# Kernel tuning notes

Measured on AMD Instinct MI355X. Metric: run time of the kernel, lower is better.

The kernel has to match this reference:

```python
import jax, jax.numpy as jnp
import numpy as np

# 5x5 neighborhood offsets as (dx, dy), row-major as in the original delta list
DELTA = [(dx, dy) for dy in (-2, -1, 0, 1, 2) for dx in (-2, -1, 0, 1, 2)]
BN_EPS = 1e-5


def _conv(x, w, padding):
    return jax.lax.conv_general_dilated(
        x, w, window_strides=(1, 1), padding=padding,
        dimension_numbers=('NCHW', 'OIHW', 'NCHW'))


def setup_inputs() -> dict:
    key = jax.random.key(0)
    ks = jax.random.split(key, 4)
    B, C, H, W = 128, 256, 24, 24
    source_feature = jax.random.normal(ks[0], (B, C, H, W), jnp.float32)
    detection_feature = jax.random.normal(ks[1], (B, C, H, W), jnp.float32)
    w1 = jax.random.normal(ks[2], (256, 512, 3, 3), jnp.float32) * 0.02
    b1 = jnp.zeros((256,), jnp.float32)
    bn_gamma = jnp.ones((256,), jnp.float32)
    bn_beta = jnp.zeros((256,), jnp.float32)
    bn_mean = jnp.zeros((256,), jnp.float32)
    bn_var = jnp.ones((256,), jnp.float32)
    w2 = jax.random.normal(ks[3], (25, 256, 1, 1), jnp.float32) * 0.05
    b2 = jnp.zeros((25,), jnp.float32)
    return dict(source_feature=source_feature, detection_feature=detection_feature,
                w1=w1, b1=b1, bn_gamma=bn_gamma, bn_beta=bn_beta,
                bn_mean=bn_mean, bn_var=bn_var, w2=w2, b2=b2)


def reference(source_feature, detection_feature, w1, b1, bn_gamma, bn_beta,
              bn_mean, bn_var, w2, b2):
    B, C, H, W = source_feature.shape
    # kernel_pre: Conv3x3(512->256, pad 1) + BN + ReLU + Conv1x1(256->25)
    concat_f = jnp.concatenate([source_feature, detection_feature], axis=1)  # [B,512,H,W]
    x = _conv(concat_f, w1, ((1, 1), (1, 1))) + b1[None, :, None, None]
    inv = bn_gamma / jnp.sqrt(bn_var + BN_EPS)
    x = x * inv[None, :, None, None] + (bn_beta - bn_mean * inv)[None, :, None, None]
    x = jax.nn.relu(x)
    logits = _conv(x, w2, ((0, 0), (0, 0))) + b2[None, :, None, None]  # [B,25,H,W]
    # per-pixel softmax over the 25 neighborhood taps
    kmaps = jax.nn.softmax(logits, axis=1)  # [B,25,H,W]
    # propagate: softmax-weighted 5x5 neighbor gather-sum; out-of-bounds taps
    # contribute zero (matches the skipped-boundary terms in the original loop)
    padded = jnp.pad(source_feature, ((0, 0), (0, 0), (2, 2), (2, 2)))
    prop = jnp.zeros_like(source_feature)
    for order, (dx, dy) in enumerate(DELTA):
        shifted = padded[:, :, 2 + dy:2 + dy + H, 2 + dx:2 + dx + W]  # [B,C,H,W]
        prop = prop + shifted * kmaps[:, order][:, None]  # broadcast over C
    return prop
```

## Files before the change

### kernel.cpp

```cpp
#include <hip/hip_runtime.h>
#include <hip/hip_bf16.h>
#include <stdint.h>

#define BATCH 128
#define CIN   256
#define CCAT  512
#define HH    24
#define WW    24
#define HP    26
#define WP    26
#define COUT  256
#define KDIM  4608
#define NPIX  576
#define MDIM  73728
#define NORD  25

typedef __attribute__((ext_vector_type(8))) short bf16x8;
typedef __attribute__((ext_vector_type(4))) float f32x4;

__device__ __forceinline__ unsigned short f2bf(float v) {
    union { float f; unsigned u; } x; x.f = v;
    unsigned r = x.u + 0x7fffu + ((x.u >> 16) & 1u);
    return (unsigned short)(r >> 16);
}
__device__ __forceinline__ float bf_lo(unsigned w) {
    union { unsigned u; float f; } x; x.u = w << 16; return x.f;
}
__device__ __forceinline__ float bf_hi(unsigned w) {
    union { unsigned u; float f; } x; x.u = w & 0xffff0000u; return x.f;
}

__device__ __forceinline__ void async_copy16(const void* gsrc, void* ldst) {
    __builtin_amdgcn_global_load_lds(
        (const __attribute__((address_space(1))) unsigned int*)gsrc,
        (__attribute__((address_space(3))) unsigned int*)ldst, 16, 0, 0);
}

#define PTILE 192
#define LSTR  72
__global__ __launch_bounds__(256) void prep_transpose(
        const float* __restrict__ src, const float* __restrict__ det,
        unsigned short* __restrict__ apad) {
    __shared__ unsigned short lds[PTILE * LSTR];
    int pt = blockIdx.x;
    int cg = blockIdx.y;
    int b  = blockIdx.z;
    int c0 = cg * 64;
    int p0 = pt * PTILE;
    const float* inp = (c0 < CIN)
        ? (src + ((long)b * CIN + c0) * NPIX)
        : (det + ((long)b * CIN + (c0 - CIN)) * NPIX);
    int tid = threadIdx.x;

    #pragma unroll
    for (int it = 0; it < 12; it++) {
        int l  = it * 256 + tid;
        int cq = l / PTILE;
        int px = l - cq * PTILE;
        const float* pb = inp + (long)cq * 4 * NPIX + p0 + px;
        unsigned short v0 = f2bf(pb[0 * NPIX]);
        unsigned short v1 = f2bf(pb[1 * NPIX]);
        unsigned short v2 = f2bf(pb[2 * NPIX]);
        unsigned short v3 = f2bf(pb[3 * NPIX]);
        uint2 w;
        w.x = (unsigned)v0 | ((unsigned)v1 << 16);
        w.y = (unsigned)v2 | ((unsigned)v3 << 16);
        *(uint2*)&lds[px * LSTR + cq * 4] = w;
    }
    __syncthreads();

    #pragma unroll
    for (int it = 0; it < 6; it++) {
        int l   = it * 256 + tid;
        int px  = l >> 3;
        int ch8 = l & 7;
        uint4 w = *(const uint4*)&lds[px * LSTR + ch8 * 8];
        int p  = p0 + px;
        int y  = p / WW, x = p - y * WW;
        long o = (((long)b * HP + (y + 1)) * WP + (x + 1)) * CCAT + c0 + ch8 * 8;
        *(uint4*)(apad + o) = w;
    }
}

__global__ __launch_bounds__(256) void zero_halo(unsigned short* __restrict__ apad) {
    int t = blockIdx.x * 256 + threadIdx.x;
    int ch8 = t & 63;
    int r   = t >> 6;
    int hp  = r % 100;
    int b   = r / 100;
    int y, x;
    if (hp < 26)      { y = 0;       x = hp; }
    else if (hp < 52) { y = 25;      x = hp - 26; }
    else if (hp < 76) { y = hp - 51; x = 0; }
    else              { y = hp - 75; x = 25; }
    long o = (((long)b * HP + y) * WP + x) * CCAT + ch8 * 8;
    *(uint4*)(apad + o) = (uint4){0u, 0u, 0u, 0u};
}

__global__ __launch_bounds__(256) void prep_w(
        const float* __restrict__ w1, const float* __restrict__ b1,
        const float* __restrict__ gam, const float* __restrict__ bet,
        const float* __restrict__ mu, const float* __restrict__ var,
        unsigned short* __restrict__ bt,
        float* __restrict__ scale, float* __restrict__ shift) {
    int idx = blockIdx.x * 256 + threadIdx.x;
    if (idx < COUT * KDIM) {
        int n = idx / KDIM;
        int k = idx - n * KDIM;
        int s = k >> 9;
        int ci = k & 511;
        int ky = s / 3, kx = s - ky * 3;
        float v = w1[(((long)n * 512 + ci) * 3 + ky) * 3 + kx];
        bt[idx] = f2bf(v);
    }
    if (blockIdx.x == 0 && threadIdx.x < COUT) {
        int c = threadIdx.x;
        float inv = gam[c] * rsqrtf(var[c] + 1e-5f);
        scale[c] = inv;
        shift[c] = (b1[c] - mu[c]) * inv + bet[c];
    }
}

#define BUF_SH  34816
#define ABUF_SH 18432
#define STAGE_A(j, nb, soff) \
    async_copy16(apad + aSrc[j] + (soff), (void*)&lds[(nb)*BUF_SH + (j)*4096 + w*512])
#define STAGE_B(j, nb, koff) \
    async_copy16(bt + bSrc[j] + (koff), (void*)&lds[(nb)*BUF_SH + ABUF_SH + (j)*4096 + w*512])
#define BAR()  __builtin_amdgcn_s_barrier()
#define WAITV4() { asm volatile("s_waitcnt vmcnt(4)" ::: "memory"); }
#define WAITV0() { asm volatile("s_waitcnt vmcnt(0)" ::: "memory"); }
#define WAITL()  { asm volatile("s_waitcnt lgkmcnt(0)" ::: "memory"); __builtin_amdgcn_sched_barrier(0); }

#define AFRAGS(mh, csw) { \
    _Pragma("unroll") \
    for (int m = 0; m < 3; m++) \
        afr[m] = *(const bf16x8*)(L + aBase + ((mh) * 3 + m) * 2048 + (csw)); }
#define BFRAGS(csw) { \
    _Pragma("unroll") \
    for (int n = 0; n < 4; n++) \
        bfr[n] = *(const bf16x8*)(L + bBase + n * 2048 + (csw)); }
#define DOMFMA(mh) { \
    __builtin_amdgcn_s_setprio(1); \
    _Pragma("unroll") \
    for (int m = 0; m < 3; m++) \
        _Pragma("unroll") \
        for (int n = 0; n < 4; n++) \
            acc[(mh) * 3 + m][n] = __builtin_amdgcn_mfma_f32_16x16x32_bf16( \
                afr[m], bfr[n], acc[(mh) * 3 + m][n], 0, 0, 0); \
    __builtin_amdgcn_s_setprio(0); }

__global__ __launch_bounds__(512, 2) void conv1_gemm(
        const unsigned short* __restrict__ apad,
        const unsigned short* __restrict__ bt,
        const float* __restrict__ scale, const float* __restrict__ shift,
        unsigned short* __restrict__ xout) {
    __shared__ unsigned short lds[2 * BUF_SH];
    const int tid  = threadIdx.x;
    const int w    = tid >> 6;
    const int lane = tid & 63;
    const int wr = w >> 2, wc = w & 3;
    const int fr = lane & 15, ls = lane >> 4;
    const long m0 = (long)blockIdx.x * 288;

    const int rowq = tid >> 3;
    const int sl   = (tid & 7) ^ (rowq & 7);
    long aSrc[5], bSrc[4];
    #pragma unroll
    for (int j = 0; j < 5; j++) {
        int r = (j == 4) ? (256 + (rowq & 31)) : (j * 64 + rowq);
        long m = m0 + r;
        int b  = (int)(m / NPIX);
        int rr = (int)(m - (long)b * NPIX);
        int y = rr / WW, x = rr - y * WW;
        aSrc[j] = (((long)b * HP + y) * WP + x) * (long)CCAT + sl * 8;
    }
    #pragma unroll
    for (int j = 0; j < 4; j++)
        bSrc[j] = (long)(j * 64 + rowq) * KDIM + sl * 8;

    const int rb   = fr & 7;
    const int csw0 = ((ls    ) ^ rb) << 4;
    const int csw1 = ((ls + 4) ^ rb) << 4;
    const int aBase = (wr * 144 + fr) * 128;
    const int bBase = ABUF_SH * 2 + (wc * 64 + fr) * 128;

    f32x4 acc[9][4];
    #pragma unroll
    for (int i = 0; i < 9; i++)
        #pragma unroll
        for (int j = 0; j < 4; j++) acc[i][j] = (f32x4){0.f, 0.f, 0.f, 0.f};

    STAGE_B(0, 0, 0); STAGE_B(1, 0, 0); STAGE_B(2, 0, 0); STAGE_B(3, 0, 0);
    STAGE_A(0, 0, 0); STAGE_A(1, 0, 0); STAGE_A(2, 0, 0); STAGE_A(3, 0, 0);
    if (tid < 256) STAGE_A(4, 0, 0);

    bf16x8 afr[3], bfr[4];
    int nb = 0;
    for (int kt = 0; kt < 71; kt++) {
        const int ktn = kt + 1;
        const int seg = ktn >> 3;
        const int ky = seg / 3, kx = seg - ky * 3;
        const long soff = (long)(ky * WP + kx) * CCAT + (ktn & 7) * 64;
        const long koff = (long)ktn * 64;
        const int pb = nb ^ 1;
        const char* L = (const char*)lds + nb * (BUF_SH * 2);

        STAGE_B(0, pb, koff); STAGE_B(1, pb, koff);
        STAGE_B(2, pb, koff); STAGE_B(3, pb, koff);
        WAITV4();
        BAR();
        BFRAGS(csw0); AFRAGS(0, csw0);
        WAITL();
        DOMFMA(0);
        BAR();

        AFRAGS(1, csw0);
        STAGE_A(0, pb, soff); STAGE_A(1, pb, soff);
        WAITL();
        DOMFMA(1);
        BAR();

        AFRAGS(2, csw0);
        STAGE_A(2, pb, soff); STAGE_A(3, pb, soff);
        if (tid < 256) STAGE_A(4, pb, soff);
        WAITL();
        DOMFMA(2);
        BAR();

        BFRAGS(csw1); AFRAGS(0, csw1);
        WAITL();
        DOMFMA(0);
        BAR();

        AFRAGS(1, csw1);
        WAITL();
        DOMFMA(1);
        BAR();

        AFRAGS(2, csw1);
        WAITL();
        DOMFMA(2);
        BAR();

        nb ^= 1;
    }

    {
        const char* L = (const char*)lds + nb * (BUF_SH * 2);
        WAITV0();
        BAR();
        BFRAGS(csw0); AFRAGS(0, csw0); WAITL(); DOMFMA(0);
        AFRAGS(1, csw0);               WAITL(); DOMFMA(1);
        AFRAGS(2, csw0);               WAITL(); DOMFMA(2);
        BFRAGS(csw1); AFRAGS(0, csw1); WAITL(); DOMFMA(0);
        AFRAGS(1, csw1);               WAITL(); DOMFMA(1);
        AFRAGS(2, csw1);               WAITL(); DOMFMA(2);
    }

    #pragma unroll
    for (int n = 0; n < 4; n++) {
        int col = wc * 64 + n * 16 + fr;
        float sc = scale[col], sh = shift[col];
        #pragma unroll
        for (int m = 0; m < 9; m++) {
            long rbase = m0 + wr * 144 + m * 16 + ls * 4;
            #pragma unroll
            for (int j = 0; j < 4; j++) {
                float v = acc[m][n][j] * sc + sh;
                v = v > 0.f ? v : 0.f;
                xout[(rbase + j) * COUT + col] = f2bf(v);
            }
        }
    }
}

__global__ __launch_bounds__(256) void conv2_softmax(
        const unsigned short* __restrict__ x, const float* __restrict__ w2,
        const float* __restrict__ b2, float* __restrict__ kmaps) {
    __shared__ float w2s[NORD * 256];
    __shared__ float b2s[NORD];
    for (int i = threadIdx.x; i < NORD * 256; i += 256) w2s[i] = w2[i];
    if (threadIdx.x < NORD) b2s[threadIdx.x] = b2[threadIdx.x];
    __syncthreads();
    long pix = (long)blockIdx.x * 256 + threadIdx.x;
    float acc[NORD];
    #pragma unroll
    for (int o = 0; o < NORD; o++) acc[o] = b2s[o];
    const unsigned short* xr = x + pix * COUT;
    for (int kc = 0; kc < 32; kc++) {
        uint4 raw = *(const uint4*)(xr + kc * 8);
        float xf[8];
        xf[0] = bf_lo(raw.x); xf[1] = bf_hi(raw.x);
        xf[2] = bf_lo(raw.y); xf[3] = bf_hi(raw.y);
        xf[4] = bf_lo(raw.z); xf[5] = bf_hi(raw.z);
        xf[6] = bf_lo(raw.w); xf[7] = bf_hi(raw.w);
        #pragma unroll
        for (int o = 0; o < NORD; o++) {
            const float* wrow = &w2s[o * 256 + kc * 8];
            float4 wa = *(const float4*)(wrow);
            float4 wb = *(const float4*)(wrow + 4);
            acc[o] += xf[0] * wa.x + xf[1] * wa.y + xf[2] * wa.z + xf[3] * wa.w
                    + xf[4] * wb.x + xf[5] * wb.y + xf[6] * wb.z + xf[7] * wb.w;
        }
    }
    float mx = acc[0];
    #pragma unroll
    for (int o = 1; o < NORD; o++) mx = fmaxf(mx, acc[o]);
    float s = 0.f;
    #pragma unroll
    for (int o = 0; o < NORD; o++) { acc[o] = expf(acc[o] - mx); s += acc[o]; }
    float inv = 1.f / s;
    #pragma unroll
    for (int o = 0; o < NORD; o++) kmaps[(long)o * MDIM + pix] = acc[o] * inv;
}

__global__ __launch_bounds__(576) void propagate(
        const float* __restrict__ src, const float* __restrict__ kmaps,
        float* __restrict__ out) {
    __shared__ float sm[4][28 * 28];
    int b  = blockIdx.y;
    int cg = blockIdx.x;
    int tid = threadIdx.x;
    int y = tid / 24, x = tid - y * 24;
    long pixg = (long)b * NPIX + tid;
    float km[NORD];
    #pragma unroll
    for (int o = 0; o < NORD; o++) km[o] = kmaps[(long)o * MDIM + pixg];
    for (int r = 0; r < 16; r++) {
        int cbase = cg * 64 + r * 4;
        __syncthreads();
        for (int t = tid; t < 4 * 784; t += 576) {
            int cp = t / 784, u = t - cp * 784;
            int yy = u / 28, xx = u - yy * 28;
            float v = 0.f;
            if (yy >= 2 && yy < 26 && xx >= 2 && xx < 26)
                v = src[((long)b * CIN + cbase + cp) * NPIX + (yy - 2) * 24 + (xx - 2)];
            sm[cp][u] = v;
        }
        __syncthreads();
        #pragma unroll
        for (int cp = 0; cp < 4; cp++) {
            float a = 0.f;
            #pragma unroll
            for (int o = 0; o < NORD; o++) {
                int dy = o / 5 - 2, dx = o % 5 - 2;
                a += km[o] * sm[cp][(y + 2 + dy) * 28 + (x + 2 + dx)];
            }
            out[((long)b * CIN + cbase + cp) * NPIX + tid] = a;
        }
    }
}

extern "C" void kernel_launch(void* const* d_in, const int* in_sizes, int n_in,
                              void* d_out, int out_size, void* d_ws, size_t ws_size,
                              hipStream_t stream) {
    const float* src = (const float*)d_in[0];
    const float* det = (const float*)d_in[1];
    const float* w1  = (const float*)d_in[2];
    const float* b1  = (const float*)d_in[3];
    const float* gam = (const float*)d_in[4];
    const float* bet = (const float*)d_in[5];
    const float* mu  = (const float*)d_in[6];
    const float* var = (const float*)d_in[7];
    const float* w2  = (const float*)d_in[8];
    const float* b2  = (const float*)d_in[9];
    float* out = (float*)d_out;

    char* ws = (char*)d_ws;
    size_t off = 0;
    unsigned short* apad = (unsigned short*)(ws + off); off += (size_t)BATCH * HP * WP * CCAT * 2;
    unsigned short* bt   = (unsigned short*)(ws + off); off += (size_t)COUT * KDIM * 2;
    unsigned short* xbuf = (unsigned short*)(ws + off); off += (size_t)MDIM * COUT * 2;
    float* kmaps = (float*)(ws + off); off += (size_t)MDIM * NORD * 4;
    float* scale = (float*)(ws + off); off += 1024;
    float* shift = (float*)(ws + off); off += 1024;

    zero_halo<<<3200, 256, 0, stream>>>(apad);
    prep_transpose<<<dim3(3, 8, BATCH), 256, 0, stream>>>(src, det, apad);
    prep_w<<<4608, 256, 0, stream>>>(w1, b1, gam, bet, mu, var, bt, scale, shift);
    conv1_gemm<<<256, 512, 0, stream>>>(apad, bt, scale, shift, xbuf);
    conv2_softmax<<<288, 256, 0, stream>>>(xbuf, w2, b2, kmaps);
    propagate<<<dim3(4, BATCH), 576, 0, stream>>>(src, kmaps, out);
}
```

Before: 345.4 us.

## Shrink conv1 GEMM tile to 96x128 and remap blocks for more parallelism

Reduces the conv1 implicit-GEMM block tile from 288x256 to 96x128, splitting N into two halves and launching 1536 blocks instead of 256. A block-index swizzle groups neighbouring M tiles and both N halves for L2 reuse, and the per-k-step pipeline drops to two MFMA phases with a smaller LDS footprint. The aim is to fill all CUs better (256 blocks underfills the MI355X) and cut register pressure, at the cost of lower arithmetic intensity per block and more global traffic for A and B reloads.

```diff
diff --git a/kernel.cpp b/kernel.cpp
--- a/kernel.cpp
+++ b/kernel.cpp
@@ -121,33 +121,33 @@
     }
 }
 
-#define BUF_SH  34816
-#define ABUF_SH 18432
+#define ABUF_SH 6144
+#define BUF_SH  14336
 #define STAGE_A(j, nb, soff) \
     async_copy16(apad + aSrc[j] + (soff), (void*)&lds[(nb)*BUF_SH + (j)*4096 + w*512])
 #define STAGE_B(j, nb, koff) \
     async_copy16(bt + bSrc[j] + (koff), (void*)&lds[(nb)*BUF_SH + ABUF_SH + (j)*4096 + w*512])
 #define BAR()  __builtin_amdgcn_s_barrier()
-#define WAITV4() { asm volatile("s_waitcnt vmcnt(4)" ::: "memory"); }
+#define WAITV2() { asm volatile("s_waitcnt vmcnt(2)" ::: "memory"); }
 #define WAITV0() { asm volatile("s_waitcnt vmcnt(0)" ::: "memory"); }
 #define WAITL()  { asm volatile("s_waitcnt lgkmcnt(0)" ::: "memory"); __builtin_amdgcn_sched_barrier(0); }
 
-#define AFRAGS(mh, csw) { \
+#define AFRAGS(csw) { \
     _Pragma("unroll") \
     for (int m = 0; m < 3; m++) \
-        afr[m] = *(const bf16x8*)(L + aBase + ((mh) * 3 + m) * 2048 + (csw)); }
+        afr[m] = *(const bf16x8*)(L + aBase + m * 2048 + (csw)); }
 #define BFRAGS(csw) { \
     _Pragma("unroll") \
-    for (int n = 0; n < 4; n++) \
+    for (int n = 0; n < 2; n++) \
         bfr[n] = *(const bf16x8*)(L + bBase + n * 2048 + (csw)); }
-#define DOMFMA(mh) { \
+#define DOMFMA() { \
     __builtin_amdgcn_s_setprio(1); \
     _Pragma("unroll") \
     for (int m = 0; m < 3; m++) \
         _Pragma("unroll") \
-        for (int n = 0; n < 4; n++) \
-            acc[(mh) * 3 + m][n] = __builtin_amdgcn_mfma_f32_16x16x32_bf16( \
-                afr[m], bfr[n], acc[(mh) * 3 + m][n], 0, 0, 0); \
+        for (int n = 0; n < 2; n++) \
+            acc[m][n] = __builtin_amdgcn_mfma_f32_16x16x32_bf16( \
+                afr[m], bfr[n], acc[m][n], 0, 0, 0); \
     __builtin_amdgcn_s_setprio(0); }
 
 __global__ __launch_bounds__(512, 2) void conv1_gemm(
@@ -161,41 +161,43 @@
     const int lane = tid & 63;
     const int wr = w >> 2, wc = w & 3;
     const int fr = lane & 15, ls = lane >> 4;
-    const long m0 = (long)blockIdx.x * 288;
+
+    const int Lb = blockIdx.x;
+    const int logical = (Lb & 7) * 192 + (Lb >> 3);
+    const int n0 = (logical & 1) * 128;
+    const long m0 = (long)(logical >> 1) * 96;
 
     const int rowq = tid >> 3;
     const int sl   = (tid & 7) ^ (rowq & 7);
-    long aSrc[5], bSrc[4];
-    #pragma unroll
-    for (int j = 0; j < 5; j++) {
-        int r = (j == 4) ? (256 + (rowq & 31)) : (j * 64 + rowq);
+    long aSrc[2], bSrc[2];
+    #pragma unroll
+    for (int j = 0; j < 2; j++) {
+        int r = (j == 0) ? rowq : (64 + (rowq & 31));
         long m = m0 + r;
         int b  = (int)(m / NPIX);
         int rr = (int)(m - (long)b * NPIX);
         int y = rr / WW, x = rr - y * WW;
         aSrc[j] = (((long)b * HP + y) * WP + x) * (long)CCAT + sl * 8;
-    }
-    #pragma unroll
-    for (int j = 0; j < 4; j++)
-        bSrc[j] = (long)(j * 64 + rowq) * KDIM + sl * 8;
+        bSrc[j] = (long)(n0 + j * 64 + rowq) * KDIM + sl * 8;
+    }
 
     const int rb   = fr & 7;
     const int csw0 = ((ls    ) ^ rb) << 4;
     const int csw1 = ((ls + 4) ^ rb) << 4;
-    const int aBase = (wr * 144 + fr) * 128;
-    const int bBase = ABUF_SH * 2 + (wc * 64 + fr) * 128;
-
-    f32x4 acc[9][4];
-    #pragma unroll
-    for (int i = 0; i < 9; i++)
+    const int aBase = (wr * 48 + fr) * 128;
+    const int bBase = ABUF_SH * 2 + (wc * 32 + fr) * 128;
+
+    f32x4 acc[3][2];
+    #pragma unroll
+    for (int i = 0; i < 3; i++)
         #pragma unroll
-        for (int j = 0; j < 4; j++) acc[i][j] = (f32x4){0.f, 0.f, 0.f, 0.f};
-
-    STAGE_B(0, 0, 0); STAGE_B(1, 0, 0); STAGE_B(2, 0, 0); STAGE_B(3, 0, 0);
-    STAGE_A(0, 0, 0); STAGE_A(1, 0, 0); STAGE_A(2, 0, 0); STAGE_A(3, 0, 0);
-    if (tid < 256) STAGE_A(4, 0, 0);
-
-    bf16x8 afr[3], bfr[4];
+        for (int j = 0; j < 2; j++) acc[i][j] = (f32x4){0.f, 0.f, 0.f, 0.f};
+
+    STAGE_B(0, 0, 0); STAGE_B(1, 0, 0);
+    STAGE_A(0, 0, 0);
+    if (tid < 256) STAGE_A(1, 0, 0);
+
+    bf16x8 afr[3], bfr[2];
     int nb = 0;
     for (int kt = 0; kt < 71; kt++) {
         const int ktn = kt + 1;
@@ -207,40 +209,18 @@
         const char* L = (const char*)lds + nb * (BUF_SH * 2);
 
         STAGE_B(0, pb, koff); STAGE_B(1, pb, koff);
-        STAGE_B(2, pb, koff); STAGE_B(3, pb, koff);
-        WAITV4();
+        WAITV2();
         BAR();
-        BFRAGS(csw0); AFRAGS(0, csw0);
+        BFRAGS(csw0); AFRAGS(csw0);
         WAITL();
-        DOMFMA(0);
+        DOMFMA();
         BAR();
 
-        AFRAGS(1, csw0);
-        STAGE_A(0, pb, soff); STAGE_A(1, pb, soff);
+        BFRAGS(csw1); AFRAGS(csw1);
+        STAGE_A(0, pb, soff);
+        if (tid < 256) STAGE_A(1, pb, soff);
         WAITL();
-        DOMFMA(1);
-        BAR();
-
-        AFRAGS(2, csw0);
-        STAGE_A(2, pb, soff); STAGE_A(3, pb, soff);
-        if (tid < 256) STAGE_A(4, pb, soff);
-        WAITL();
-        DOMFMA(2);
-        BAR();
-
-        BFRAGS(csw1); AFRAGS(0, csw1);
-        WAITL();
-        DOMFMA(0);
-        BAR();
-
-        AFRAGS(1, csw1);
-        WAITL();
-        DOMFMA(1);
-        BAR();
-
-        AFRAGS(2, csw1);
-        WAITL();
-        DOMFMA(2);
+        DOMFMA();
         BAR();
 
         nb ^= 1;
@@ -250,21 +230,17 @@
         const char* L = (const char*)lds + nb * (BUF_SH * 2);
         WAITV0();
         BAR();
-        BFRAGS(csw0); AFRAGS(0, csw0); WAITL(); DOMFMA(0);
-        AFRAGS(1, csw0);               WAITL(); DOMFMA(1);
-        AFRAGS(2, csw0);               WAITL(); DOMFMA(2);
-        BFRAGS(csw1); AFRAGS(0, csw1); WAITL(); DOMFMA(0);
-        AFRAGS(1, csw1);               WAITL(); DOMFMA(1);
-        AFRAGS(2, csw1);               WAITL(); DOMFMA(2);
-    }
-
-    #pragma unroll
-    for (int n = 0; n < 4; n++) {
-        int col = wc * 64 + n * 16 + fr;
+        BFRAGS(csw0); AFRAGS(csw0); WAITL(); DOMFMA();
+        BFRAGS(csw1); AFRAGS(csw1); WAITL(); DOMFMA();
+    }
+
+    #pragma unroll
+    for (int n = 0; n < 2; n++) {
+        int col = n0 + wc * 32 + n * 16 + fr;
         float sc = scale[col], sh = shift[col];
         #pragma unroll
-        for (int m = 0; m < 9; m++) {
-            long rbase = m0 + wr * 144 + m * 16 + ls * 4;
+        for (int m = 0; m < 3; m++) {
+            long rbase = m0 + wr * 48 + m * 16 + ls * 4;
             #pragma unroll
             for (int j = 0; j < 4; j++) {
                 float v = acc[m][n][j] * sc + sh;
@@ -379,7 +355,7 @@
     zero_halo<<<3200, 256, 0, stream>>>(apad);
     prep_transpose<<<dim3(3, 8, BATCH), 256, 0, stream>>>(src, det, apad);
     prep_w<<<4608, 256, 0, stream>>>(w1, b1, gam, bet, mu, var, bt, scale, shift);
-    conv1_gemm<<<256, 512, 0, stream>>>(apad, bt, scale, shift, xbuf);
+    conv1_gemm<<<1536, 512, 0, stream>>>(apad, bt, scale, shift, xbuf);
     conv2_softmax<<<288, 256, 0, stream>>>(xbuf, w2, b2, kmaps);
     propagate<<<dim3(4, BATCH), 576, 0, stream>>>(src, kmaps, out);
 }
```

New measurement: 369.3 us. 1.07x slower.
